# Kernel optimization log

Hardware: AMD Instinct MI355X
Metric: run time of the kernel (lower is better)

Reference implementation:

```python
import jax, jax.numpy as jnp
import numpy as np

LAMBDA_SOFTMAX = 9.0
LAMBDA_LSE = 6.0
MARGIN = 0.2
EPS = 1e-8
NEG = -1e9


def setup_inputs() -> dict:
    key = jax.random.key(0)
    k1, k2, k3 = jax.random.split(key, 3)
    B, R, L, D = 128, 36, 48, 1024
    images = jax.random.normal(k1, (B, R, D), dtype=jnp.float32)
    captions = jax.random.normal(k2, (B, L, D), dtype=jnp.float32)
    cap_lens = jax.random.randint(k3, (B,), L // 2, L + 1, dtype=jnp.int32)
    # zero out padded words (original slices captions[:, :n_word], so padding never enters)
    wmask = (jnp.arange(L)[None, :] < cap_lens[:, None]).astype(jnp.float32)
    captions = captions * wmask[:, :, None]
    return {"images": images, "captions": captions, "cap_lens": cap_lens}


def _safe_norm_sq(q):
    # sqrt with guarded input so padded (all-zero) rows don't produce inf grads
    return jnp.sqrt(jnp.clip(q, 1e-16, None))


def _l2norm(x, axis):
    # matches l2norm: x / (sqrt(sum x^2) + eps)
    return x / (jnp.sqrt(jnp.sum(x * x, axis=axis, keepdims=True)) + EPS)


def _focal_renorm(attn, sourceL):
    # focal_equal: keep entries whose prob exceeds the row mean, then renormalize
    s = jnp.sum(attn, axis=-1, keepdims=True)
    fattn = (attn * sourceL - s > 0).astype(attn.dtype)
    tmp = fattn * attn
    ts = jnp.sum(tmp, axis=-1, keepdims=True)
    return tmp / jnp.where(ts > 0, ts, 1.0)


def reference(images, captions, cap_lens):
    C, L, D = captions.shape
    I, R, _ = images.shape
    wmask = (jnp.arange(L)[None, :] < cap_lens[:, None]).astype(captions.dtype)  # [C,L]
    caps = captions * wmask[:, :, None]
    nw = cap_lens.astype(captions.dtype)  # ragged sourceL for i2t focal

    # shared raw dot products: [C, I, L, R]
    dots = jnp.einsum('cld,ird->cilr', caps, images)

    # Gram matrices to get |weightedContext| without materializing [.,.,.,D] tensors
    img_gram = jnp.einsum('ird,isd->irs', images, images)   # [I,R,R]
    cap_gram = jnp.einsum('cld,cmd->clm', caps, caps)       # [C,L,L]
    cap_norm = _safe_norm_sq(jnp.sum(caps * caps, -1))      # [C,L]
    img_norm = _safe_norm_sq(jnp.sum(images * images, -1))  # [I,R]

    # ---------- t2i: query = caption words, context = image regions ----------
    a = jax.nn.leaky_relu(dots, 0.1)                 # raw attn (context x query^T), [C,I,L,R]
    a = _l2norm(a, axis=2)                           # l2norm over query words (dim=2 in [b,sourceL,queryL])
    a = jax.nn.softmax(a * LAMBDA_SOFTMAX, axis=-1)  # softmax over regions
    re_t = _focal_renorm(a, float(R))                # [C,I,L,R]
    # cosine(cap_word, weightedContext): w12 = sum_r re*dots; |wctx|^2 via image Gram
    w12 = jnp.sum(re_t * dots, axis=-1)                                   # [C,I,L]
    w2 = _safe_norm_sq(jnp.einsum('cilr,cils,irs->cil', re_t, re_t, img_gram))
    t2i_sim = w12 / jnp.clip(cap_norm[:, None, :] * w2, EPS, None)        # [C,I,L]
    # LogSumExp aggregation over valid words only
    t2i = jnp.log(jnp.sum(wmask[:, None, :] * jnp.exp(LAMBDA_LSE * t2i_sim), -1)) / LAMBDA_LSE  # [C,I]

    # ---------- i2t: query = image regions, context = caption words ----------
    b = jax.nn.leaky_relu(dots, 0.1)
    b = _l2norm(b, axis=3)                           # l2norm over regions (dim=2 in [b,L,R])
    logits = jnp.where(wmask[:, None, :, None] > 0, b * LAMBDA_SOFTMAX, NEG)
    b = jax.nn.softmax(logits, axis=2)               # softmax over valid words
    # focal over words, axis=2; sourceL = actual caption length (ragged)
    s = jnp.sum(b, axis=2, keepdims=True)
    fattn = (b * nw[:, None, None, None] - s > 0).astype(b.dtype)
    tmp = fattn * b
    ts = jnp.sum(tmp, axis=2, keepdims=True)
    re_i = tmp / jnp.where(ts > 0, ts, 1.0)          # [C,I,L,R]
    w12i = jnp.sum(re_i * dots, axis=2)                                   # [C,I,R]
    w2i = _safe_norm_sq(jnp.einsum('cilr,cimr,clm->cir', re_i, re_i, cap_gram))
    i2t_sim = w12i / jnp.clip(img_norm[None, :, :] * w2i, EPS, None)      # [C,I,R]
    i2t = jnp.log(jnp.sum(jnp.exp(LAMBDA_LSE * i2t_sim), -1)) / LAMBDA_LSE  # [C,I]

    scores = (t2i + i2t).T  # [n_image, n_caption]

    # ---------- margin-based ranking loss (max_violation) ----------
    d = jnp.diagonal(scores)
    cost_s = jnp.clip(MARGIN + scores - d[:, None], 0.0, None)
    cost_im = jnp.clip(MARGIN + scores - d[None, :], 0.0, None)
    eye = jnp.eye(scores.shape[0], dtype=bool)
    cost_s = jnp.where(eye, 0.0, cost_s)
    cost_im = jnp.where(eye, 0.0, cost_im)
    loss = jnp.sum(jnp.max(cost_s, axis=1)) + jnp.sum(jnp.max(cost_im, axis=0))
    return loss
```

## Files before the change

kernel.cpp:

```cpp
#include <hip/hip_runtime.h>
#include <math.h>

#define CN 128
#define INN 128
#define LN 48
#define RN 36
#define DN 1024
#define RTA 36
#define MT 6144
#define NT 4608
#define EPSF 1e-8f
#define LSM 9.0f
#define LLSE 6.0f
#define LOG2E 1.4426950408889634f

__device__ __forceinline__ float leaky(float x){ return x > 0.f ? x : 0.1f*x; }

typedef const __attribute__((address_space(1))) unsigned int* gp_t;
typedef __attribute__((address_space(3))) unsigned int* lp_t;
__device__ __forceinline__ void gload16u(const ushort* g, ushort* l) {
  __builtin_amdgcn_global_load_lds((gp_t)g, (lp_t)l, 16, 0, 0);
}

typedef short s16x8 __attribute__((ext_vector_type(8)));
typedef float f32x4 __attribute__((ext_vector_type(4)));

__device__ __forceinline__ ushort bf16rne(float f) {
  const unsigned u = __float_as_uint(f);
  return (ushort)((u + 0x7fffu + ((u>>16)&1u)) >> 16);
}
__device__ __forceinline__ float bf2f(ushort u) {
  return __uint_as_float((unsigned)u << 16);
}
__device__ __forceinline__ int swzi(int row, int col) {
  return (col & 7) | ((((col >> 3) ^ (row & 7)) & 7) << 3);
}

__global__ __launch_bounds__(256) void conv_kernel(
    const float* __restrict__ caps, const float* __restrict__ imgs,
    ushort* __restrict__ aHi, ushort* __restrict__ bHi)
{
  const int NA = MT*DN/4, NB = NT*DN/4;
  for (int i = blockIdx.x*256 + threadIdx.x; i < NA + NB; i += gridDim.x*256) {
    const float4 v = (i < NA) ? ((const float4*)caps)[i] : ((const float4*)imgs)[i - NA];
    const ushort4 h = make_ushort4(bf16rne(v.x), bf16rne(v.y), bf16rne(v.z), bf16rne(v.w));
    if (i < NA) ((ushort4*)aHi)[i] = h;
    else        ((ushort4*)bHi)[i-NA] = h;
  }
}

__global__ __launch_bounds__(256) void gram_mfma_kernel(
    const ushort* __restrict__ aHi, const ushort* __restrict__ bHi,
    float* __restrict__ nI, float* __restrict__ nC,
    ushort* __restrict__ gIb, ushort* __restrict__ gCb)
{
  __shared__ __align__(16) ushort sX[48*64];
  const int b = blockIdx.x, tid = threadIdx.x;
  const bool isImg = b < INN;
  const int R = isImg ? RN : LN;
  const ushort* X = isImg ? (bHi + (size_t)b*RN*DN) : (aHi + (size_t)(b-INN)*LN*DN);
  ushort* gOut = isImg ? (gIb + (size_t)b*3072) : (gCb + (size_t)(b-INN)*3072);
  float* nOut = isImg ? (nI + b*RN) : (nC + (b-INN)*LN);
  const int lane = tid & 63, wv = tid >> 6;
  const int l15 = lane & 15, kg = lane >> 4;

  f32x4 acc[3];
  #pragma unroll
  for (int i = 0; i < 3; ++i) acc[i] = (f32x4){0.f,0.f,0.f,0.f};

  for (int k0 = 0; k0 < DN; k0 += 64) {
    __syncthreads();
    for (int idx = tid; idx < R*8; idx += 256) {
      const int row = idx >> 3, gp = idx & 7;
      *(uint4*)&sX[row*64 + (gp ^ (row&7))*8] =
        *(const uint4*)(X + (size_t)row*DN + k0 + gp*8);
    }
    __syncthreads();
    #pragma unroll
    for (int i = 0; i < 3; ++i) {
      const int tt = wv + 4*i;
      if (tt < 9) {
        const int mt = tt/3, nt = tt - 3*(tt/3);
        #pragma unroll
        for (int ks = 0; ks < 2; ++ks) {
          const int rA = mt*16 + l15, rB = nt*16 + l15;
          const s16x8 af = *(const s16x8*)&sX[rA*64 + (((ks*4+kg) ^ (rA&7)))*8];
          const s16x8 bf = *(const s16x8*)&sX[rB*64 + (((ks*4+kg) ^ (rB&7)))*8];
          acc[i] = __builtin_amdgcn_mfma_f32_16x16x32_bf16(af, bf, acc[i], 0,0,0);
        }
      }
    }
  }
  #pragma unroll
  for (int i = 0; i < 3; ++i) {
    const int tt = wv + 4*i;
    if (tt < 9) {
      const int mt = tt/3, nt = tt - 3*(tt/3);
      #pragma unroll
      for (int rg = 0; rg < 4; ++rg) {
        const int m = mt*16 + kg*4 + rg, n = nt*16 + l15;
        const float cv = acc[i][rg];
        gOut[m*64 + n] = (m < R && n < R) ? bf16rne(cv) : (ushort)0;
        if (m == n && m < R) nOut[m] = sqrtf(fmaxf(cv, 1e-16f));
      }
    }
  }
  for (int idx = tid; idx < 48*16; idx += 256) {
    const int row = idx >> 4, col = 48 + (idx & 15);
    gOut[row*64 + col] = 0;
  }
}

__global__ __launch_bounds__(256) void dots_gemm_mfma(
    const ushort* __restrict__ aHi, const ushort* __restrict__ bHi,
    float* __restrict__ dots, int arow0)
{
  __shared__ __align__(16) ushort sT[16384];
  const int tid = threadIdx.x;
  const int wv = tid >> 6, lane = tid & 63;
  const int l15 = lane & 15, kg = lane >> 4;
  const int wr = wv >> 1, wc = wv & 1;
  const int M0 = blockIdx.y * 128;
  const int N0 = blockIdx.x * 128;

  int offA[4], offB[4];
  #pragma unroll
  for (int f = 0; f < 4; ++f) {
    offA[f] = (wr*64 + f*16 + l15)*64;
    offB[f] = (wc*64 + f*16 + l15)*64;
  }
  int srow[4], sgk[4]; unsigned dOff[4];
  #pragma unroll
  for (int h = 0; h < 4; ++h) {
    const int ch = h*256 + tid;
    const int row = ch >> 3, gp = ch & 7;
    srow[h] = row;
    sgk[h] = (gp ^ (row & 7)) * 8;
    dOff[h] = (unsigned)(h*256 + wv*64) * 8;
  }

  f32x4 acc[4][4];
  #pragma unroll
  for (int mf = 0; mf < 4; ++mf)
    #pragma unroll
    for (int nf = 0; nf < 4; ++nf) acc[mf][nf] = (f32x4){0.f,0.f,0.f,0.f};

  const size_t aR = (size_t)(arow0 + M0);
  for (int k0 = 0; k0 < DN; k0 += 64) {
    __syncthreads();
    #pragma unroll
    for (int h = 0; h < 4; ++h) {
      const size_t ao = (aR + srow[h])*DN + k0 + sgk[h];
      const size_t bo = ((size_t)(N0 + srow[h]))*DN + k0 + sgk[h];
      gload16u(aHi + ao, sT + dOff[h]);
      gload16u(bHi + bo, sT + 8192 + dOff[h]);
    }
    asm volatile("s_waitcnt vmcnt(0)" ::: "memory");
    __syncthreads();
    #pragma unroll
    for (int ks = 0; ks < 2; ++ks) {
      s16x8 ah[4], bh[4];
      #pragma unroll
      for (int f = 0; f < 4; ++f) {
        const int rA = wr*64 + f*16 + l15;
        const int rB = wc*64 + f*16 + l15;
        ah[f] = *(const s16x8*)&sT[offA[f] + (((ks*4+kg) ^ (rA&7)))*8];
        bh[f] = *(const s16x8*)&sT[8192 + offB[f] + (((ks*4+kg) ^ (rB&7)))*8];
      }
      #pragma unroll
      for (int mf = 0; mf < 4; ++mf)
        #pragma unroll
        for (int nf = 0; nf < 4; ++nf)
          acc[mf][nf] = __builtin_amdgcn_mfma_f32_16x16x32_bf16(ah[mf], bh[nf], acc[mf][nf], 0,0,0);
    }
  }
  #pragma unroll
  for (int mf = 0; mf < 4; ++mf)
    #pragma unroll
    for (int nf = 0; nf < 4; ++nf) {
      const int n = N0 + wc*64 + nf*16 + l15;
      #pragma unroll
      for (int r = 0; r < 4; ++r) {
        const int m = M0 + wr*64 + mf*16 + kg*4 + r;
        dots[(size_t)m*NT + n] = acc[mf][nf][r];
      }
    }
}

__global__ __launch_bounds__(256) void attn_kernel(
    const float* __restrict__ dots, const int* __restrict__ cap_lens,
    const ushort* __restrict__ gIb, const ushort* __restrict__ gCb,
    const float* __restrict__ nI, const float* __restrict__ nC,
    float* __restrict__ scores, int cbase)
{
  __shared__ float sDots[LN][RTA+1];
  __shared__ __align__(16) ushort sMeT[LN*64];
  __shared__ __align__(16) ushort sMeIT[48*64];
  __shared__ float sQqT[LN], sQqI[48];
  __shared__ float sW12t[LN], sInvT[LN];
  __shared__ float sW12i[RN], sInvI[RN];
  __shared__ float sColInv[RN], sRowInv[LN];
  __shared__ float sCapN[LN], sImgN[RN];
  __shared__ float sEt[LN], sEi[RN];
  __shared__ float sRed[2];

  const int cl = blockIdx.y;
  const int c  = cbase + cl;
  const int it = blockIdx.x;
  const int tid = threadIdx.x;
  const int lane = tid & 63, wv = tid >> 6;
  const int l15 = lane & 15, kg = lane >> 4;
  const int team = tid >> 2, q4 = tid & 3;
  const int nw = cap_lens[c];
  const float nwf = (float)nw;

  for (int idx = tid; idx < LN*RTA/4; idx += 256) {
    const int l = idx / (RTA/4), jseg = idx - l*(RTA/4);
    const float4 v = *(const float4*)(dots + ((size_t)cl*LN + l)*NT + (size_t)it*RTA + jseg*4);
    float* dst = &sDots[l][jseg*4];
    dst[0]=v.x; dst[1]=v.y; dst[2]=v.z; dst[3]=v.w;
  }
  for (int idx = tid; idx < 768; idx += 256) {
    if (idx < 384) ((uint4*)sMeT)[idx] = make_uint4(0,0,0,0);
    else ((uint4*)sMeIT)[idx-384] = make_uint4(0,0,0,0);
  }
  if (tid < LN) { sCapN[tid] = nC[c*LN + tid]; sQqT[tid] = 0.f; }
  if (tid >= 64 && tid < 64+48) sQqI[tid-64] = 0.f;
  if (tid >= 128 && tid < 128+RN) sImgN[tid-128] = nI[it*RN + (tid-128)];
  __syncthreads();

  #pragma unroll 1
  for (int pass = 0; pass < 2; ++pass) {
    const int vrow = pass*64 + team;
    if (vrow < RN) {
      float s = 0.f;
      #pragma unroll
      for (int j = 0; j < 12; ++j) { const float v = leaky(sDots[q4*12+j][vrow]); s += v*v; }
      s += __shfl_xor(s, 1, 4); s += __shfl_xor(s, 2, 4);
      if (q4 == 0) sColInv[vrow] = (LSM*LOG2E) * __builtin_amdgcn_rcpf(sqrtf(s) + EPSF);
    } else if (vrow < RN + LN) {
      const int l = vrow - RN;
      float s = 0.f;
      #pragma unroll
      for (int j = 0; j < 9; ++j) { const float v = leaky(sDots[l][q4*9+j]); s += v*v; }
      s += __shfl_xor(s, 1, 4); s += __shfl_xor(s, 2, 4);
      if (q4 == 0) sRowInv[l] = (LSM*LOG2E) * __builtin_amdgcn_rcpf(sqrtf(s) + EPSF);
    }
  }
  __syncthreads();

  #pragma unroll 1
  for (int pass = 0; pass < 2; ++pass) {
    const int vrow = pass*64 + team;
    if (vrow < LN) {
      const int l = vrow;
      const int cb = q4*9;
      float d9[9], x9[9];
      #pragma unroll
      for (int j = 0; j < 9; ++j) d9[j] = sDots[l][cb + j];
      float se = 0.f;
      #pragma unroll
      for (int j = 0; j < 9; ++j) {
        const float e = exp2f(leaky(d9[j]) * sColInv[cb + j]);
        x9[j] = e; se += e;
      }
      se += __shfl_xor(se, 1, 4); se += __shfl_xor(se, 2, 4);
      float ts = 0.f;
      #pragma unroll
      for (int j = 0; j < 9; ++j) {
        const float me = (x9[j]*36.f > se) ? x9[j] : 0.f;
        x9[j] = me; ts += me;
      }
      ts += __shfl_xor(ts, 1, 4); ts += __shfl_xor(ts, 2, 4);
      float w12 = 0.f;
      #pragma unroll
      for (int j = 0; j < 9; ++j) w12 += x9[j]*d9[j];
      w12 += __shfl_xor(w12, 1, 4); w12 += __shfl_xor(w12, 2, 4);
      #pragma unroll
      for (int j = 0; j < 9; ++j)
        sMeT[l*64 + swzi(l, cb + j)] = bf16rne(x9[j]);
      if (q4 == 0) {
        sW12t[l] = w12;
        sInvT[l] = __builtin_amdgcn_rcpf((ts > 0.f) ? ts : 1.f);
      }
    } else {
      const int r = vrow - LN;
      if (r < RN) {
        float d12[12], x12[12];
        #pragma unroll
        for (int j = 0; j < 12; ++j) d12[j] = sDots[q4*12+j][r];
        float se = 0.f;
        #pragma unroll
        for (int j = 0; j < 12; ++j) {
          const int l = q4*12 + j;
          const float e = (l < nw) ? exp2f(leaky(d12[j]) * sRowInv[l]) : 0.f;
          x12[j] = e; se += e;
        }
        se += __shfl_xor(se, 1, 4); se += __shfl_xor(se, 2, 4);
        float ts = 0.f;
        #pragma unroll
        for (int j = 0; j < 12; ++j) {
          const float me = (x12[j]*nwf > se) ? x12[j] : 0.f;
          x12[j] = me; ts += me;
        }
        ts += __shfl_xor(ts, 1, 4); ts += __shfl_xor(ts, 2, 4);
        float w12 = 0.f;
        #pragma unroll
        for (int j = 0; j < 12; ++j) w12 += x12[j]*d12[j];
        w12 += __shfl_xor(w12, 1, 4); w12 += __shfl_xor(w12, 2, 4);
        #pragma unroll
        for (int j = 0; j < 12; ++j)
          sMeIT[r*64 + swzi(r, q4*12 + j)] = bf16rne(x12[j]);
        if (q4 == 0) {
          sW12i[r] = w12;
          sInvI[r] = __builtin_amdgcn_rcpf((ts > 0.f) ? ts : 1.f);
        }
      }
    }
  }
  __syncthreads();

  const ushort* gIbase = gIb + (size_t)it*3072;
  const ushort* gCbase = gCb + (size_t)c*3072;
  #pragma unroll 1
  for (int t = wv; t < 18; t += 4) {
    const bool isT = (t < 9);
    const int tt = isT ? t : t - 9;
    const int mt = tt / 3, nt = tt - 3*(tt/3);
    const ushort* Ab = isT ? gIbase : gCbase;
    const ushort* Mb = isT ? sMeT   : sMeIT;
    const int arow = mt*16 + l15;
    const int brow = nt*16 + l15;
    f32x4 acc = (f32x4){0.f,0.f,0.f,0.f};
    #pragma unroll
    for (int ks = 0; ks < 2; ++ks) {
      const s16x8 af = *(const s16x8*)(Ab + arow*64 + (ks*4+kg)*8);
      const s16x8 bf = *(const s16x8*)&Mb[brow*64 + (((ks*4+kg) ^ (brow&7)))*8];
      acc = __builtin_amdgcn_mfma_f32_16x16x32_bf16(af, bf, acc, 0,0,0);
    }
    float part = 0.f;
    #pragma unroll
    for (int rg = 0; rg < 4; ++rg) {
      const int orow = mt*16 + kg*4 + rg;
      part += acc[rg] * bf2f(Mb[brow*64 + swzi(brow, orow)]);
    }
    part += __shfl_xor(part, 16);
    part += __shfl_xor(part, 32);
    if (lane < 16)
      atomicAdd(isT ? &sQqT[nt*16 + l15] : &sQqI[nt*16 + l15], part);
  }
  __syncthreads();

  if (tid < LN) {
    const float invd = sInvT[tid];
    const float w2 = sqrtf(fmaxf(sQqT[tid]*invd*invd, 1e-16f));
    const float sim = (sW12t[tid]*invd) * __builtin_amdgcn_rcpf(fmaxf(sCapN[tid]*w2, EPSF));
    sEt[tid] = (tid < nw) ? exp2f((LLSE*LOG2E)*sim) : 0.f;
  }
  if (tid >= 64 && tid < 64+RN) {
    const int r = tid - 64;
    const float invd = sInvI[r];
    const float w2 = sqrtf(fmaxf(sQqI[r]*invd*invd, 1e-16f));
    const float sim = (sW12i[r]*invd) * __builtin_amdgcn_rcpf(fmaxf(sImgN[r]*w2, EPSF));
    sEi[r] = exp2f((LLSE*LOG2E)*sim);
  }
  __syncthreads();
  if (wv == 0) {
    float e = (lane < LN) ? sEt[lane] : 0.f;
    #pragma unroll
    for (int o = 32; o > 0; o >>= 1) e += __shfl_xor(e, o);
    if (lane == 0) sRed[0] = e;
  } else if (wv == 1) {
    float e = (lane < RN) ? sEi[lane] : 0.f;
    #pragma unroll
    for (int o = 32; o > 0; o >>= 1) e += __shfl_xor(e, o);
    if (lane == 0) sRed[1] = e;
  }
  __syncthreads();
  if (tid == 0)
    scores[(size_t)it*CN + c] = log2f(sRed[0]*sRed[1]) * (1.f/(LLSE*LOG2E));
}

__global__ __launch_bounds__(128) void loss_kernel(
    const float* __restrict__ S, float* __restrict__ out)
{
  __shared__ float red[128];
  const int t = threadIdx.x;
  const float d = S[t*CN + t];
  float m1 = -1e30f, m2 = -1e30f;
  for (int cc = 0; cc < CN; ++cc)
    if (cc != t) m1 = fmaxf(m1, 0.2f + S[t*CN+cc] - d);
  for (int i2 = 0; i2 < INN; ++i2)
    if (i2 != t) m2 = fmaxf(m2, 0.2f + S[i2*CN+t] - d);
  red[t] = fmaxf(m1, 0.f) + fmaxf(m2, 0.f);
  __syncthreads();
  for (int s = 64; s > 0; s >>= 1) {
    if (t < s) red[t] += red[t+s];
    __syncthreads();
  }
  if (t == 0) out[0] = red[0];
}

extern "C" void kernel_launch(void* const* d_in, const int* in_sizes, int n_in,
                              void* d_out, int out_size, void* d_ws, size_t ws_size,
                              hipStream_t stream) {
  (void)in_sizes; (void)n_in; (void)out_size;
  const float* imgs = (const float*)d_in[0];
  const float* caps = (const float*)d_in[1];
  const int*   lens = (const int*)d_in[2];

  const size_t bfUS = 2*((size_t)MT + NT)*DN;
  const size_t gbUS = (size_t)(INN + CN)*3072;
  const size_t smallF = (size_t)INN*RN*RN + INN*RN + (size_t)CN*LN*LN + CN*LN + (size_t)INN*CN;
  int g = CN;
  while (g > 8) {
    const size_t need = (bfUS + gbUS)*2 + (smallF + (size_t)g*LN*NT)*4;
    if (need <= ws_size) break;
    g >>= 1;
  }

  ushort* aHi = (ushort*)d_ws;
  ushort* aLo = aHi + (size_t)MT*DN;
  ushort* bHi = aLo + (size_t)MT*DN;
  ushort* bLo = bHi + (size_t)NT*DN;
  ushort* gIb = bLo + (size_t)NT*DN;
  ushort* gCb = gIb + (size_t)INN*3072;
  float* fbase = (float*)(gCb + (size_t)CN*3072);
  float* gI     = fbase;
  float* nI     = gI + (size_t)INN*RN*RN;
  float* gC     = nI + (size_t)INN*RN;
  float* nC     = gC + (size_t)CN*LN*LN;
  float* scores = nC + (size_t)CN*LN;
  float* dots   = scores + (size_t)INN*CN;

  conv_kernel<<<dim3(1024), dim3(256), 0, stream>>>(caps, imgs, aHi, bHi);
  gram_mfma_kernel<<<dim3(INN+CN), dim3(256), 0, stream>>>(
      aHi, bHi, nI, nC, gIb, gCb);
  for (int c0 = 0; c0 < CN; c0 += g) {
    dots_gemm_mfma<<<dim3(NT/128, g*LN/128), dim3(256), 0, stream>>>(
        aHi, bHi, dots, c0*LN);
    attn_kernel<<<dim3(INN, g), dim3(256), 0, stream>>>(
        dots, lens, gIb, gCb, nI, nC, scores, c0);
  }
  loss_kernel<<<dim3(1), dim3(128), 0, stream>>>(scores, (float*)d_out);
}
```

Measured before the change: 250.2 us.

## Double-buffer LDS tiles in dots GEMM with K-step of 32

The bf16 MFMA GEMM producing the caption-image dot products now splits shared memory into two 32-wide K buffers. It issues the global-to-LDS loads for the next K slice before running the MFMAs on the current one, where previously it loaded 64-wide slices synchronously. The swizzle pattern is adapted to the 32-column rows. The aim is to hide global load latency behind compute, at the cost of twice as many barriers per K and smaller per-iteration work.

```diff
diff --git a/kernel.cpp b/kernel.cpp
--- a/kernel.cpp
+++ b/kernel.cpp
@@ -115,7 +115,7 @@
     const ushort* __restrict__ aHi, const ushort* __restrict__ bHi,
     float* __restrict__ dots, int arow0)
 {
-  __shared__ __align__(16) ushort sT[16384];
+  __shared__ __align__(16) ushort sT[2][8192];
   const int tid = threadIdx.x;
   const int wv = tid >> 6, lane = tid & 63;
   const int l15 = lane & 15, kg = lane >> 4;
@@ -126,16 +126,18 @@
   int offA[4], offB[4];
   #pragma unroll
   for (int f = 0; f < 4; ++f) {
-    offA[f] = (wr*64 + f*16 + l15)*64;
-    offB[f] = (wc*64 + f*16 + l15)*64;
-  }
-  int srow[4], sgk[4]; unsigned dOff[4];
-  #pragma unroll
-  for (int h = 0; h < 4; ++h) {
-    const int ch = h*256 + tid;
-    const int row = ch >> 3, gp = ch & 7;
+    const int rA = wr*64 + f*16 + l15;
+    offA[f] = rA*32 + ((kg ^ ((rA>>1)&3)) << 3);
+    const int rB = wc*64 + f*16 + l15;
+    offB[f] = rB*32 + ((kg ^ ((rB>>1)&3)) << 3);
+  }
+  int srow[2], sgk[2]; unsigned dOff[2];
+  #pragma unroll
+  for (int h = 0; h < 2; ++h) {
+    const int ch = h*256 + wv*64 + lane;
+    const int row = ch >> 2, gp = ch & 3;
     srow[h] = row;
-    sgk[h] = (gp ^ (row & 7)) * 8;
+    sgk[h] = (gp ^ ((row>>1)&3)) * 8;
     dOff[h] = (unsigned)(h*256 + wv*64) * 8;
   }
 
@@ -146,33 +148,39 @@
     for (int nf = 0; nf < 4; ++nf) acc[mf][nf] = (f32x4){0.f,0.f,0.f,0.f};
 
   const size_t aR = (size_t)(arow0 + M0);
-  for (int k0 = 0; k0 < DN; k0 += 64) {
-    __syncthreads();
-    #pragma unroll
-    for (int h = 0; h < 4; ++h) {
-      const size_t ao = (aR + srow[h])*DN + k0 + sgk[h];
-      const size_t bo = ((size_t)(N0 + srow[h]))*DN + k0 + sgk[h];
-      gload16u(aHi + ao, sT + dOff[h]);
-      gload16u(bHi + bo, sT + 8192 + dOff[h]);
-    }
+
+  #pragma unroll
+  for (int h = 0; h < 2; ++h) {
+    gload16u(aHi + (aR + srow[h])*DN + sgk[h],                  &sT[0][0]    + dOff[h]);
+    gload16u(bHi + ((size_t)(N0 + srow[h]))*DN + sgk[h],        &sT[0][4096] + dOff[h]);
+  }
+  asm volatile("s_waitcnt vmcnt(0)" ::: "memory");
+  __syncthreads();
+
+  int cur = 0;
+  for (int t = 0; t < 32; ++t) {
+    if (t < 31) {
+      const int k1 = (t + 1) * 32;
+      #pragma unroll
+      for (int h = 0; h < 2; ++h) {
+        gload16u(aHi + (aR + srow[h])*DN + k1 + sgk[h],           &sT[cur^1][0]    + dOff[h]);
+        gload16u(bHi + ((size_t)(N0 + srow[h]))*DN + k1 + sgk[h], &sT[cur^1][4096] + dOff[h]);
+      }
+    }
+    s16x8 ah[4], bh[4];
+    #pragma unroll
+    for (int f = 0; f < 4; ++f) {
+      ah[f] = *(const s16x8*)&sT[cur][offA[f]];
+      bh[f] = *(const s16x8*)&sT[cur][4096 + offB[f]];
+    }
+    #pragma unroll
+    for (int mf = 0; mf < 4; ++mf)
+      #pragma unroll
+      for (int nf = 0; nf < 4; ++nf)
+        acc[mf][nf] = __builtin_amdgcn_mfma_f32_16x16x32_bf16(ah[mf], bh[nf], acc[mf][nf], 0,0,0);
     asm volatile("s_waitcnt vmcnt(0)" ::: "memory");
     __syncthreads();
-    #pragma unroll
-    for (int ks = 0; ks < 2; ++ks) {
-      s16x8 ah[4], bh[4];
-      #pragma unroll
-      for (int f = 0; f < 4; ++f) {
-        const int rA = wr*64 + f*16 + l15;
-        const int rB = wc*64 + f*16 + l15;
-        ah[f] = *(const s16x8*)&sT[offA[f] + (((ks*4+kg) ^ (rA&7)))*8];
-        bh[f] = *(const s16x8*)&sT[8192 + offB[f] + (((ks*4+kg) ^ (rB&7)))*8];
-      }
-      #pragma unroll
-      for (int mf = 0; mf < 4; ++mf)
-        #pragma unroll
-        for (int nf = 0; nf < 4; ++nf)
-          acc[mf][nf] = __builtin_amdgcn_mfma_f32_16x16x32_bf16(ah[mf], bh[nf], acc[mf][nf], 0,0,0);
-    }
+    cur ^= 1;
   }
   #pragma unroll
   for (int mf = 0; mf < 4; ++mf)
```

Measured after the change: 248.3 us. Within noise of the previous version (-0.7%).
